# Optimization experiments

Hardware: AMD Instinct MI355X
Metric: run time of the kernel (lower is better)

## Reference

```python
import jax, jax.numpy as jnp
import numpy as np

KSIZE = 3
COUT = 128
GC = 4

def _unfold(x, k):
    # x: [B,C,H,W] -> [B,C,k*k,H,W]; zero pad (k-1)//2, stride 1 (matches nn.Unfold ordering)
    B, C, H, W = x.shape
    p = (k - 1) // 2
    xp = jnp.pad(x, ((0, 0), (0, 0), (p, p), (p, p)))
    return jnp.stack([xp[:, :, i:i + H, j:j + W] for i in range(k) for j in range(k)], axis=2)

def _bn(x, g, b, m, v, eps=1e-5):
    # inference-mode BatchNorm along channel axis 1, any rank
    sh = (1, -1) + (1,) * (x.ndim - 2)
    return (x - m.reshape(sh)) * (g / jnp.sqrt(v + eps)).reshape(sh) + b.reshape(sh)

def setup_inputs():
    key = jax.random.key(0)
    ks = jax.random.split(key, 15)
    B, C, H, W = 4, 128, 56, 56
    mid = C // 4
    OG = COUT * GC
    s = 0.05
    return {
        'x': jax.random.normal(ks[0], (B, C, H, W), jnp.float32),
        'Wk': jax.random.normal(ks[1], (C, C), jnp.float32) * s,
        'bn1_g': jax.random.uniform(ks[2], (C,), jnp.float32, 0.5, 1.5),
        'bn1_b': jax.random.normal(ks[3], (C,), jnp.float32) * s,
        'bn1_m': jnp.zeros((C,), jnp.float32),
        'bn1_v': jnp.ones((C,), jnp.float32),
        'W1': jax.random.normal(ks[4], (mid, 2 * C), jnp.float32) * s,
        'b1': jax.random.normal(ks[5], (mid,), jnp.float32) * s,
        'bn2_g': jax.random.uniform(ks[6], (mid,), jnp.float32, 0.5, 1.5),
        'bn2_b': jax.random.normal(ks[7], (mid,), jnp.float32) * s,
        'bn2_m': jnp.zeros((mid,), jnp.float32),
        'bn2_v': jnp.ones((mid,), jnp.float32),
        'W2': jax.random.normal(ks[8], (OG, mid), jnp.float32) * s,
        'b2': jax.random.normal(ks[9], (OG,), jnp.float32) * s,
        'gn_g': jax.random.uniform(ks[10], (OG,), jnp.float32, 0.5, 1.5),
        'gn_b': jax.random.normal(ks[11], (OG,), jnp.float32) * s,
        'Wv': jax.random.normal(ks[12], (OG, C), jnp.float32) * s,
        'bnv_g': jax.random.uniform(ks[13], (OG,), jnp.float32, 0.5, 1.5),
        'bnv_b': jax.random.normal(ks[14], (OG,), jnp.float32) * s,
        'bnv_m': jnp.zeros((OG,), jnp.float32),
        'bnv_v': jnp.ones((OG,), jnp.float32),
    }

def reference(x, Wk, bn1_g, bn1_b, bn1_m, bn1_v, W1, b1, bn2_g, bn2_b, bn2_m, bn2_v,
              W2, b2, gn_g, gn_b, Wv, bnv_g, bnv_b, bnv_m, bnv_v):
    B, C, H, W = x.shape
    k2 = KSIZE * KSIZE
    # emb_K: 1x1 conv (no bias) + BN + ReLU, then local unfold
    ke = jax.nn.relu(_bn(jnp.einsum('bchw,dc->bdhw', x, Wk), bn1_g, bn1_b, bn1_m, bn1_v))
    Kp = _unfold(ke, KSIZE)                        # [B,C,k2,H,W]
    Q = jnp.broadcast_to(x[:, :, None], Kp.shape)  # repeat x over k2 (einops '(c k)')
    QK = jnp.concatenate([Q, Kp], axis=1)          # [B,2C,k2,H,W]
    # MLP: 1x1 convs act pointwise over (k2,H,W)
    h = jax.nn.relu(_bn(jnp.einsum('bcphw,mc->bmphw', QK, W1) + b1.reshape(1, -1, 1, 1, 1),
                        bn2_g, bn2_b, bn2_m, bn2_v))
    a = jnp.einsum('bmphw,om->bophw', h, W2) + b2.reshape(1, -1, 1, 1, 1)  # [B,COUT*GC,k2,H,W]
    a = a.reshape(B, COUT, GC, k2, H, W)
    # GroupNorm: num_groups=COUT -> normalize over (GC, k2, H, W) per (b, out)
    mu = a.mean(axis=(2, 3, 4, 5), keepdims=True)
    var = jnp.mean(jnp.square(a - mu), axis=(2, 3, 4, 5), keepdims=True)
    a = (a - mu) / jnp.sqrt(var + 1e-5)
    a = a * gn_g.reshape(1, COUT, GC, 1, 1, 1) + gn_b.reshape(1, COUT, GC, 1, 1, 1)
    # emb_V: 1x1 conv (no bias) + BN, then local unfold
    v = _bn(jnp.einsum('bchw,oc->bohw', x, Wv), bnv_g, bnv_b, bnv_m, bnv_v)
    V = _unfold(v, KSIZE).reshape(B, COUT, GC, k2, H, W)
    return jnp.sum(a * V, axis=(2, 3))             # [B,COUT,H,W]
```

## Files before the change

### kernel.cpp

```cpp
#include <hip/hip_runtime.h>
#include <hip/hip_bf16.h>

typedef __hip_bfloat16 bf16;
typedef __attribute__((ext_vector_type(8))) short short8;
typedef __attribute__((ext_vector_type(4))) float f32x4;

#define HWP 3136
#define WD 56
#define PW 58
#define PADP 3364
#define CC 128
#define MIDM 32
#define OGN 512
#define NB 4

enum : int {
  OFF_FLAG = 0,
  OFF_W2F  = 4,
  OFF_SC2  = OFF_W2F + OGN*MIDM,
  OFF_SH2  = OFF_SC2 + MIDM,
  OFF_B1F  = OFF_SH2 + MIDM,
  OFF_B2F  = OFF_B1F + MIDM,
  OFF_GNG  = OFF_B2F + OGN,
  OFF_GNB  = OFF_GNG + OGN,
  OFF_GPART= OFF_GNB + OGN,
  OFF_PQ   = OFF_GPART + NB*128*1056,
  OFF_SS1  = OFF_PQ + NB*OGN*2,
  OFF_SSV  = OFF_SS1 + CC*2,
  OFF_WKB  = OFF_SSV + OGN*2,
  OFF_WVB  = OFF_WKB + CC*CC/2,
  OFF_W1AB = OFF_WVB + OGN*CC/2,
  OFF_W1BB = OFF_W1AB + MIDM*CC/2,
  OFF_HQT  = OFF_W1BB + MIDM*CC/2,
  OFF_GKT  = OFF_HQT + NB*HWP*MIDM/2,
  OFF_VT   = OFF_GKT + NB*PADP*MIDM/2,
  OFF_R1   = OFF_VT + NB*PADP*OGN/2,
  OFF_XT   = OFF_R1,
  OFF_AB   = OFF_R1,
  WS_TOTAL = OFF_R1 + NB*9*HWP*MIDM/2
};

__device__ __forceinline__ float b2f(unsigned short u) {
  bf16 h; *(unsigned short*)&h = u; return __bfloat162float(h);
}
__device__ __forceinline__ unsigned short f2b(float f) {
  bf16 h = __float2bfloat16(f); return *(unsigned short*)&h;
}
__device__ __forceinline__ float ldmix(const void* p, size_t i, bool isbf) {
  return isbf ? __bfloat162float(((const bf16*)p)[i]) : ((const float*)p)[i];
}
__device__ __forceinline__ f32x4 mfma16(short8 a, short8 b, f32x4 c) {
  return __builtin_amdgcn_mfma_f32_16x16x32_bf16(a, b, c, 0, 0, 0);
}
__device__ __forceinline__ bool detect_bf(const unsigned short* xr) {
  int cnt = 0;
#pragma unroll
  for (int i = 0; i < 32; i++) {
    short8 v = *(const short8*)(xr + i*8);
#pragma unroll
    for (int j = 0; j < 8; j++) {
      int e = (((unsigned short)v[j]) >> 7) & 0xFF;
      cnt += (e >= 141) ? 1 : 0;
    }
  }
  return cnt < 8;
}

__global__ __launch_bounds__(256) void k_prep(
    const void* __restrict__ x,  const void* __restrict__ Wk,
    const void* __restrict__ bn1_g, const void* __restrict__ bn1_b,
    const void* __restrict__ bn1_m, const void* __restrict__ bn1_v,
    const void* __restrict__ W1, const void* __restrict__ b1,
    const void* __restrict__ bn2_g, const void* __restrict__ bn2_b,
    const void* __restrict__ bn2_m, const void* __restrict__ bn2_v,
    const void* __restrict__ W2, const void* __restrict__ b2,
    const void* __restrict__ gn_g, const void* __restrict__ gn_b,
    const void* __restrict__ Wv,
    const void* __restrict__ bnv_g, const void* __restrict__ bnv_b,
    const void* __restrict__ bnv_m, const void* __restrict__ bnv_v,
    float* __restrict__ ws) {
  __shared__ unsigned short tile[32*130];
  const bool isbf = detect_bf((const unsigned short*)x);
  int blk = blockIdx.x, tid = threadIdx.x;
  if (blk == 0 && tid == 0) ws[OFF_FLAG] = isbf ? 1.f : 0.f;
  int gid = blk*256 + tid, gstride = gridDim.x*256;
  unsigned short* wkb = (unsigned short*)(ws + OFF_WKB);
  unsigned short* wvb = (unsigned short*)(ws + OFF_WVB);
  unsigned short* w1ab = (unsigned short*)(ws + OFF_W1AB);
  unsigned short* w1bb = (unsigned short*)(ws + OFF_W1BB);
  float2* ss1 = (float2*)(ws + OFF_SS1);
  float2* ssv = (float2*)(ws + OFF_SSV);
  for (int i = gid; i < CC*CC; i += gstride) wkb[i] = f2b(ldmix(Wk, i, isbf));
  for (int i = gid; i < OGN*CC; i += gstride) wvb[i] = f2b(ldmix(Wv, i, isbf));
  for (int i = gid; i < MIDM*CC; i += gstride) {
    int m = i / CC, c = i % CC;
    w1ab[i] = f2b(ldmix(W1, (size_t)m*(2*CC) + c, isbf));
    w1bb[i] = f2b(ldmix(W1, (size_t)m*(2*CC) + CC + c, isbf));
  }
  for (int i = gid; i < OGN*MIDM; i += gstride) ws[OFF_W2F + i] = ldmix(W2, i, isbf);
  for (int i = gid; i < CC; i += gstride) {
    float s = ldmix(bn1_g, i, isbf) / sqrtf(ldmix(bn1_v, i, isbf) + 1e-5f);
    ss1[i] = make_float2(s, ldmix(bn1_b, i, isbf) - ldmix(bn1_m, i, isbf) * s);
  }
  for (int i = gid; i < MIDM; i += gstride) {
    float s = ldmix(bn2_g, i, isbf) / sqrtf(ldmix(bn2_v, i, isbf) + 1e-5f);
    ws[OFF_SC2 + i] = s;
    ws[OFF_SH2 + i] = ldmix(bn2_b, i, isbf) - ldmix(bn2_m, i, isbf)*s;
    ws[OFF_B1F + i] = ldmix(b1, i, isbf);
  }
  for (int i = gid; i < OGN; i += gstride) {
    float s = ldmix(bnv_g, i, isbf) / sqrtf(ldmix(bnv_v, i, isbf) + 1e-5f);
    ssv[i] = make_float2(s, ldmix(bnv_b, i, isbf) - ldmix(bnv_m, i, isbf) * s);
    ws[OFF_B2F + i] = ldmix(b2, i, isbf);
    ws[OFF_GNG + i] = ldmix(gn_g, i, isbf);
    ws[OFF_GNB + i] = ldmix(gn_b, i, isbf);
  }
  if (blk < 392) {
    int b = blk / 98, pix0 = (blk % 98)*32;
#pragma unroll
    for (int k = 0; k < 16; k++) {
      int idx = tid + k*256;
      int c = idx >> 5, pl = idx & 31;
      tile[pl*130 + c] = f2b(ldmix(x, ((size_t)b*CC + c)*HWP + pix0 + pl, isbf));
    }
    __syncthreads();
    unsigned short* xt = (unsigned short*)(ws + OFF_XT);
#pragma unroll
    for (int k = 0; k < 16; k++) {
      int idx = tid + k*256;
      int c = idx & 127, pl = idx >> 7;
      xt[((size_t)b*HWP + pix0 + pl)*CC + c] = tile[pl*130 + c];
    }
  } else {
    const int NV = 912*64, NG = NB*PADP*4;
    const short8 z = {0,0,0,0,0,0,0,0};
    unsigned short* vt = (unsigned short*)(ws + OFF_VT);
    unsigned short* gk = (unsigned short*)(ws + OFF_GKT);
    for (int u = (blk-392)*256 + tid; u < NV + NG; u += 28*256) {
      if (u < NV) {
        int bpp = u >> 6, och = u & 63;
        int b = bpp / 228, j = bpp - b*228;
        int pp;
        if (j < 58)       pp = j;
        else if (j < 116) pp = 57*PW + (j - 58);
        else if (j < 172) pp = (j - 116 + 1)*PW;
        else              pp = (j - 172 + 1)*PW + 57;
        *(short8*)(vt + ((size_t)b*PADP + pp)*OGN + och*8) = z;
      } else {
        int u2 = u - NV;
        int b = u2 / (PADP*4), rem = u2 - b*(PADP*4);
        int pp = rem >> 2, mch = rem & 3;
        *(short8*)(gk + ((size_t)b*PADP + pp)*MIDM + mch*8) = z;
      }
    }
  }
}

__global__ __launch_bounds__(256, 4) void k_mid(float* __restrict__ ws) {
  __shared__ unsigned short keL[4][16][136];
  int bid = blockIdx.x, tid = threadIdx.x;
  int w = tid >> 6, lane = tid & 63, q = lane >> 4, l16 = lane & 15;
  if (bid < 196) {
    int b = bid / 49, bx = bid - (bid/49)*49;
    int pix = bx*64 + w*16 + l16;
    const unsigned short* xt = (const unsigned short*)(ws + OFF_XT) + ((size_t)b*HWP + pix)*CC;
    short8 Bx[4];
#pragma unroll
    for (int kk = 0; kk < 4; kk++) Bx[kk] = *(const short8*)(xt + kk*32 + q*8);
    const unsigned short* wkb = (const unsigned short*)(ws + OFF_WKB);
    const float2* ss = (const float2*)(ws + OFF_SS1);
#pragma unroll
    for (int ot = 0; ot < 8; ot++) {
      int drow = ot*16 + l16;
      f32x4 c = {0.f, 0.f, 0.f, 0.f};
#pragma unroll
      for (int kk = 0; kk < 4; kk++)
        c = mfma16(*(const short8*)(wkb + (size_t)drow*CC + kk*32 + q*8), Bx[kk], c);
      int d0 = ot*16 + q*4;
      ushort4 st;
      { float2 s = ss[d0+0]; st.x = f2b(fmaxf(s.x*c[0] + s.y, 0.f)); }
      { float2 s = ss[d0+1]; st.y = f2b(fmaxf(s.x*c[1] + s.y, 0.f)); }
      { float2 s = ss[d0+2]; st.z = f2b(fmaxf(s.x*c[2] + s.y, 0.f)); }
      { float2 s = ss[d0+3]; st.w = f2b(fmaxf(s.x*c[3] + s.y, 0.f)); }
      *(ushort4*)&keL[w][l16][d0] = st;
    }
    __syncthreads();
    short8 Bk[4];
#pragma unroll
    for (int kk = 0; kk < 4; kk++) Bk[kk] = *(const short8*)&keL[w][l16][kk*32 + q*8];
    const unsigned short* w1a = (const unsigned short*)(ws + OFF_W1AB);
    const unsigned short* w1b = (const unsigned short*)(ws + OFF_W1BB);
    int h0 = pix / WD, w0 = pix - h0*WD;
    int pp = (h0+1)*PW + (w0+1);
    unsigned short* hqt = (unsigned short*)(ws + OFF_HQT) + ((size_t)b*HWP + pix)*MIDM;
    unsigned short* gkt = (unsigned short*)(ws + OFF_GKT) + ((size_t)b*PADP + pp)*MIDM;
#pragma unroll
    for (int mt = 0; mt < 2; mt++) {
      int mrow = mt*16 + l16;
      f32x4 ch = {0.f,0.f,0.f,0.f}, cg = {0.f,0.f,0.f,0.f};
#pragma unroll
      for (int kk = 0; kk < 4; kk++) {
        ch = mfma16(*(const short8*)(w1a + (size_t)mrow*CC + kk*32 + q*8), Bx[kk], ch);
        cg = mfma16(*(const short8*)(w1b + (size_t)mrow*CC + kk*32 + q*8), Bk[kk], cg);
      }
      int m0 = mt*16 + q*4;
      ushort4 sh, sg;
      sh.x = f2b(ch[0]); sh.y = f2b(ch[1]); sh.z = f2b(ch[2]); sh.w = f2b(ch[3]);
      sg.x = f2b(cg[0]); sg.y = f2b(cg[1]); sg.z = f2b(cg[2]); sg.w = f2b(cg[3]);
      *(ushort4*)(hqt + m0) = sh;
      *(ushort4*)(gkt + m0) = sg;
    }
  } else {
    int vid = bid - 196;
    int bx = vid % 49, rest = vid / 49;
    int by = rest & 3, b = rest >> 2;
    int pix = bx*64 + w*16 + l16;
    int h0 = pix / WD, w0 = pix - h0*WD;
    int pp = (h0+1)*PW + (w0+1);
    const unsigned short* xt = (const unsigned short*)(ws + OFF_XT) + ((size_t)b*HWP + pix)*CC;
    short8 B[4];
#pragma unroll
    for (int kk = 0; kk < 4; kk++) B[kk] = *(const short8*)(xt + kk*32 + q*8);
    const unsigned short* wvb = (const unsigned short*)(ws + OFF_WVB);
    const float2* ss = (const float2*)(ws + OFF_SSV);
    unsigned short* vt = (unsigned short*)(ws + OFF_VT) + ((size_t)b*PADP + pp)*OGN;
#pragma unroll
    for (int ot = 0; ot < 8; ot++) {
      int orow = by*128 + ot*16 + l16;
      f32x4 c = {0.f, 0.f, 0.f, 0.f};
#pragma unroll
      for (int kk = 0; kk < 4; kk++)
        c = mfma16(*(const short8*)(wvb + (size_t)orow*CC + kk*32 + q*8), B[kk], c);
      int o0 = by*128 + ot*16 + q*4;
      ushort4 st;
      { float2 s = ss[o0+0]; st.x = f2b(s.x*c[0] + s.y); }
      { float2 s = ss[o0+1]; st.y = f2b(s.x*c[1] + s.y); }
      { float2 s = ss[o0+2]; st.z = f2b(s.x*c[2] + s.y); }
      { float2 s = ss[o0+3]; st.w = f2b(s.x*c[3] + s.y); }
      *(ushort4*)(vt + o0) = st;
    }
  }
}

__global__ __launch_bounds__(256) void k_gramh(float* __restrict__ ws) {
  __shared__ unsigned short tileT[32][264];
  int b = blockIdx.y, bk = blockIdx.x;
  int tid = threadIdx.x;
  int w = tid >> 6, lane = tid & 63, q = lane >> 4, l16 = lane & 15;
  const int base = bk * 882;
  const unsigned short* hqt = (const unsigned short*)(ws + OFF_HQT) + (size_t)b*HWP*MIDM;
  const unsigned short* gkp = (const unsigned short*)(ws + OFF_GKT) + (size_t)b*PADP*MIDM;
  float sc2[MIDM], bas0[MIDM];
#pragma unroll
  for (int m = 0; m < MIDM; m++) {
    sc2[m] = ws[OFF_SC2 + m];
    bas0[m] = sc2[m]*ws[OFF_B1F + m] + ws[OFF_SH2 + m];
  }
  f32x4 gLL={0,0,0,0}, gLH={0,0,0,0}, gHH={0,0,0,0}, sL={0,0,0,0}, sH={0,0,0,0};
  short8 ones;
#pragma unroll
  for (int j = 0; j < 8; j++) ones[j] = (short)0x3F80;
  for (int t = 0; t < 4; t++) {
    int r = t*256 + tid;
    bool valid = r < 882;
    int R = valid ? (base + r) : 0;
    int p = R / HWP, pix = R - p*HWP;
    int h0 = pix / WD, w0 = pix - h0*WD;
    int npp = (h0 + p/3)*PW + (w0 + p - (p/3)*3);
    const unsigned short* hq = hqt + (size_t)pix*MIDM;
    const unsigned short* gk = gkp + (size_t)npp*MIDM;
#pragma unroll
    for (int ch = 0; ch < 4; ch++) {
      short8 th = *(const short8*)(hq + ch*8);
      short8 tg = *(const short8*)(gk + ch*8);
      short8 o;
#pragma unroll
      for (int j = 0; j < 8; j++) {
        int m = ch*8 + j;
        float hv = b2f((unsigned short)th[j]) + b2f((unsigned short)tg[j]);
        float v = fmaxf(sc2[m]*hv + bas0[m], 0.f);
        o[j] = valid ? (short)f2b(v) : (short)0;
      }
#pragma unroll
      for (int j = 0; j < 8; j++) tileT[ch*8 + j][tid] = (unsigned short)o[j];
    }
    __syncthreads();
#pragma unroll
    for (int cc = 0; cc < 2; cc++) {
      int c = w*2 + cc;
      short8 alo = *(const short8*)&tileT[l16][c*32 + q*8];
      short8 ahi = *(const short8*)&tileT[l16+16][c*32 + q*8];
      gLL = mfma16(alo, alo, gLL);
      gLH = mfma16(alo, ahi, gLH);
      gHH = mfma16(ahi, ahi, gHH);
      sL = mfma16(alo, ones, sL);
      sH = mfma16(ahi, ones, sH);
    }
    __syncthreads();
  }
  float* blob = ws + OFF_GPART + ((size_t)((b*32 + bk)*4 + w))*1056;
#pragma unroll
  for (int r = 0; r < 4; r++) {
    int row = q*4 + r;
    blob[row*32 + l16]             = gLL[r];
    blob[row*32 + 16 + l16]        = gLH[r];
    blob[(16 + l16)*32 + row]      = gLH[r];
    blob[(16 + row)*32 + 16 + l16] = gHH[r];
  }
  if (l16 == 0) {
#pragma unroll
    for (int r = 0; r < 4; r++) {
      blob[1024 + q*4 + r]      = sL[r];
      blob[1024 + 16 + q*4 + r] = sH[r];
    }
  }
}

__global__ __launch_bounds__(512) void k_stats(float* __restrict__ ws) {
  __shared__ float Gs[MIDM*MIDM], S1s[MIDM], saS[OGN], sqS[OGN], muS[128], invS[128];
  int b = blockIdx.x, o = threadIdx.x;
  for (int e = o; e < 1056; e += 512) {
    float s = 0.f;
    const float* pb = ws + OFF_GPART + (size_t)b*128*1056 + e;
    for (int p = 0; p < 128; p++) s += pb[(size_t)p*1056];
    if (e < 1024) Gs[e] = s; else S1s[e - 1024] = s;
  }
  __syncthreads();
  float w2[MIDM];
#pragma unroll
  for (int m = 0; m < MIDM; m++) w2[m] = ws[OFF_W2F + o*MIDM + m];
  float dotS = 0.f;
#pragma unroll
  for (int m = 0; m < MIDM; m++) dotS += w2[m] * S1s[m];
  float quad = 0.f;
  for (int a = 0; a < MIDM; a++) {
    float t = 0.f;
#pragma unroll
    for (int c = 0; c < MIDM; c++) t += Gs[a*MIDM + c] * w2[c];
    quad += w2[a] * t;
  }
  float b2o = ws[OFF_B2F + o];
  const float M = 9.f * HWP;
  saS[o] = dotS + b2o * M;
  sqS[o] = quad + 2.f*b2o*dotS + b2o*b2o*M;
  __syncthreads();
  if (o < 128) {
    float sa = saS[4*o] + saS[4*o+1] + saS[4*o+2] + saS[4*o+3];
    float sq = sqS[4*o] + sqS[4*o+1] + sqS[4*o+2] + sqS[4*o+3];
    const float invN = 1.f / (4.f * M);
    float mu = sa * invN;
    float var = sq * invN - mu*mu;
    muS[o] = mu;
    invS[o] = 1.f / sqrtf(var + 1e-5f);
  }
  __syncthreads();
  int co = o >> 2;
  float alpha = ws[OFF_GNG + o] * invS[co];
  ((float2*)(ws + OFF_PQ))[b*OGN + o] =
      make_float2(alpha, alpha*b2o + ws[OFF_GNB + o] - muS[co]*alpha);
  unsigned short* dst = (unsigned short*)(ws + OFF_AB) + ((size_t)b*OGN + o)*MIDM;
#pragma unroll
  for (int m = 0; m < MIDM; m += 4) {
    ushort4 t;
    t.x = f2b(alpha*w2[m+0]); t.y = f2b(alpha*w2[m+1]);
    t.z = f2b(alpha*w2[m+2]); t.w = f2b(alpha*w2[m+3]);
    *(ushort4*)(dst + m) = t;
  }
}

#define VST 136
__global__ __launch_bounds__(256, 2) void k_out(const float* __restrict__ ws,
                                                void* __restrict__ outp) {
  __shared__ unsigned short tileV[256*VST];
  int b = blockIdx.z, bp = blockIdx.y;
  int bx = blockIdx.x;
  int tid = threadIdx.x;
  int w = tid >> 6, lane = tid & 63, q = lane >> 4, l16 = lane & 15;
  int pix0 = bx*128;
  int h00 = pix0 / WD, w00 = pix0 - h00*WD;
  int wstart = (h00+1)*PW + (w00+1) - (PW+1);
  const bool hasB = (bx < 24);
  int pixA = pix0 + w*16 + l16;
  float sc[8], ba[8];
#pragma unroll
  for (int j = 0; j < 8; j++) {
    int m = q*8 + j;
    sc[j] = ws[OFF_SC2 + m];
    ba[j] = sc[j]*ws[OFF_B1F + m] + ws[OFF_SH2 + m];
  }
  const unsigned short* hqt = (const unsigned short*)(ws + OFF_HQT) + (size_t)b*HWP*MIDM;
  const unsigned short* gkt = (const unsigned short*)(ws + OFF_GKT) + (size_t)b*PADP*MIDM;
  int hA = pixA / WD, wA = pixA - hA*WD;
  short8 BfA[9];
  {
    short8 th = *(const short8*)(hqt + (size_t)pixA*MIDM + q*8);
    float hv[8];
#pragma unroll
    for (int j = 0; j < 8; j++) hv[j] = b2f((unsigned short)th[j]);
    const unsigned short* gkb = gkt + ((size_t)hA*PW + wA)*MIDM + q*8;
#pragma unroll
    for (int p = 0; p < 9; p++) {
      short8 tg = *(const short8*)(gkb + (size_t)((p/3)*PW + (p - (p/3)*3))*MIDM);
#pragma unroll
      for (int j = 0; j < 8; j++)
        BfA[p][j] = (short)f2b(fmaxf(sc[j]*(hv[j] + b2f((unsigned short)tg[j])) + ba[j], 0.f));
    }
  }
  const unsigned short* vsrc = (const unsigned short*)(ws + OFF_VT)
      + (size_t)b*PADP*OGN + (size_t)bp*128;
#pragma unroll
  for (int i = 0; i < 16; i++) {
    int u = i*256 + tid;
    int wp = u >> 4, col = (u & 15)*8;
    *(short8*)&tileV[wp*VST + col] =
        *(const short8*)(vsrc + (size_t)(wstart + wp)*OGN + col);
  }
  const bool isbf = ws[OFF_FLAG] > 0.5f;
  const float2* pq = (const float2*)(ws + OFF_PQ) + b*OGN;
  const unsigned short* ABb = (const unsigned short*)(ws + OFF_AB)
      + ((size_t)b*OGN + bp*128)*MIDM;
  const int doff[9] = {-PW-1, -PW, -PW+1, -1, 0, 1, PW-1, PW, PW+1};
  int pplA = (hA+1)*PW + (wA+1) - wstart;
  __syncthreads();
  for (int byv = 0; byv < 2; ++byv) {
    short8 A[4];
    f32x4 Qv[4];
#pragma unroll
    for (int ot = 0; ot < 4; ot++) {
      A[ot] = *(const short8*)(ABb + (size_t)(byv*64 + ot*16 + l16)*MIDM + q*8);
      int o0 = bp*128 + byv*64 + ot*16 + q*4;
      f32x4 qv = { pq[o0+0].y, pq[o0+1].y, pq[o0+2].y, pq[o0+3].y };
      Qv[ot] = qv;
    }
    {
      float acc[4] = {0.f, 0.f, 0.f, 0.f};
#pragma unroll
      for (int p = 0; p < 9; p++) {
        int lp = pplA + doff[p];
        const unsigned short* vrow = &tileV[lp*VST + byv*64];
#pragma unroll
        for (int ot = 0; ot < 4; ot++) {
          f32x4 c = {0.f, 0.f, 0.f, 0.f};
          c = mfma16(A[ot], BfA[p], c);
          ushort4 vv = *(const ushort4*)(vrow + ot*16 + q*4);
          acc[ot] += (c[0] + Qv[ot][0])*b2f(vv.x) + (c[1] + Qv[ot][1])*b2f(vv.y)
                   + (c[2] + Qv[ot][2])*b2f(vv.z) + (c[3] + Qv[ot][3])*b2f(vv.w);
        }
      }
#pragma unroll
      for (int ot = 0; ot < 4; ot++) {
        int co = bp*32 + byv*16 + ot*4 + q;
        size_t oidx = ((size_t)b*128 + co)*HWP + pixA;
        if (isbf) __builtin_nontemporal_store(f2b(acc[ot]), (unsigned short*)outp + oidx);
        else      __builtin_nontemporal_store(acc[ot], (float*)outp + oidx);
      }
    }
    if (hasB) {
      int pixB = pixA + 64;
      int hB = pixB / WD, wB = pixB - hB*WD;
      short8 BfB[9];
      {
        short8 th = *(const short8*)(hqt + (size_t)pixB*MIDM + q*8);
        float hv[8];
#pragma unroll
        for (int j = 0; j < 8; j++) hv[j] = b2f((unsigned short)th[j]);
        const unsigned short* gkb = gkt + ((size_t)hB*PW + wB)*MIDM + q*8;
#pragma unroll
        for (int p = 0; p < 9; p++) {
          short8 tg = *(const short8*)(gkb + (size_t)((p/3)*PW + (p - (p/3)*3))*MIDM);
#pragma unroll
          for (int j = 0; j < 8; j++)
            BfB[p][j] = (short)f2b(fmaxf(sc[j]*(hv[j] + b2f((unsigned short)tg[j])) + ba[j], 0.f));
        }
      }
      int ppl = (hB+1)*PW + (wB+1) - wstart;
      float acc[4] = {0.f, 0.f, 0.f, 0.f};
#pragma unroll
      for (int p = 0; p < 9; p++) {
        int lp = ppl + doff[p];
        const unsigned short* vrow = &tileV[lp*VST + byv*64];
#pragma unroll
        for (int ot = 0; ot < 4; ot++) {
          f32x4 c = {0.f, 0.f, 0.f, 0.f};
          c = mfma16(A[ot], BfB[p], c);
          ushort4 vv = *(const ushort4*)(vrow + ot*16 + q*4);
          acc[ot] += (c[0] + Qv[ot][0])*b2f(vv.x) + (c[1] + Qv[ot][1])*b2f(vv.y)
                   + (c[2] + Qv[ot][2])*b2f(vv.z) + (c[3] + Qv[ot][3])*b2f(vv.w);
        }
      }
#pragma unroll
      for (int ot = 0; ot < 4; ot++) {
        int co = bp*32 + byv*16 + ot*4 + q;
        size_t oidx = ((size_t)b*128 + co)*HWP + pixB;
        if (isbf) __builtin_nontemporal_store(f2b(acc[ot]), (unsigned short*)outp + oidx);
        else      __builtin_nontemporal_store(acc[ot], (float*)outp + oidx);
      }
    }
  }
}

extern "C" void kernel_launch(void* const* d_in, const int* in_sizes, int n_in,
                              void* d_out, int out_size, void* d_ws, size_t ws_size,
                              hipStream_t stream) {
  float* ws = (float*)d_ws;
  hipLaunchKernelGGL(k_prep, dim3(420), dim3(256), 0, stream,
                     d_in[0], d_in[1], d_in[2], d_in[3], d_in[4], d_in[5],
                     d_in[6], d_in[7], d_in[8], d_in[9], d_in[10], d_in[11],
                     d_in[12], d_in[13], d_in[14], d_in[15], d_in[16],
                     d_in[17], d_in[18], d_in[19], d_in[20], ws);
  hipLaunchKernelGGL(k_mid,  dim3(980),      dim3(256), 0, stream, ws);
  hipLaunchKernelGGL(k_gramh,dim3(32, 4),    dim3(256), 0, stream, ws);
  hipLaunchKernelGGL(k_stats,dim3(4),        dim3(512), 0, stream, ws);
  hipLaunchKernelGGL(k_out,  dim3(25, 4, 4), dim3(256), 0, stream, ws, d_out);
}
```

Baseline: 192.9 us.

## Fuse V projection into output kernel instead of materializing padded V

Result: slower. 201.7 us (+4.5%).

```diff
diff --git a/kernel.cpp b/kernel.cpp
--- a/kernel.cpp
+++ b/kernel.cpp
@@ -33,11 +33,9 @@
   OFF_W1BB = OFF_W1AB + MIDM*CC/2,
   OFF_HQT  = OFF_W1BB + MIDM*CC/2,
   OFF_GKT  = OFF_HQT + NB*HWP*MIDM/2,
-  OFF_VT   = OFF_GKT + NB*PADP*MIDM/2,
-  OFF_R1   = OFF_VT + NB*PADP*OGN/2,
-  OFF_XT   = OFF_R1,
-  OFF_AB   = OFF_R1,
-  WS_TOTAL = OFF_R1 + NB*9*HWP*MIDM/2
+  OFF_AB   = OFF_GKT + NB*PADP*MIDM/2,
+  OFF_XT   = OFF_AB + NB*OGN*MIDM/2,
+  WS_TOTAL = OFF_XT + NB*HWP*CC/2
 };
 
 __device__ __forceinline__ float b2f(unsigned short u) {
@@ -132,26 +130,13 @@
       xt[((size_t)b*HWP + pix0 + pl)*CC + c] = tile[pl*130 + c];
     }
   } else {
-    const int NV = 912*64, NG = NB*PADP*4;
+    const int NG = NB*PADP*4;
     const short8 z = {0,0,0,0,0,0,0,0};
-    unsigned short* vt = (unsigned short*)(ws + OFF_VT);
     unsigned short* gk = (unsigned short*)(ws + OFF_GKT);
-    for (int u = (blk-392)*256 + tid; u < NV + NG; u += 28*256) {
-      if (u < NV) {
-        int bpp = u >> 6, och = u & 63;
-        int b = bpp / 228, j = bpp - b*228;
-        int pp;
-        if (j < 58)       pp = j;
-        else if (j < 116) pp = 57*PW + (j - 58);
-        else if (j < 172) pp = (j - 116 + 1)*PW;
-        else              pp = (j - 172 + 1)*PW + 57;
-        *(short8*)(vt + ((size_t)b*PADP + pp)*OGN + och*8) = z;
-      } else {
-        int u2 = u - NV;
-        int b = u2 / (PADP*4), rem = u2 - b*(PADP*4);
-        int pp = rem >> 2, mch = rem & 3;
-        *(short8*)(gk + ((size_t)b*PADP + pp)*MIDM + mch*8) = z;
-      }
+    for (int u = (blk-392)*256 + tid; u < NG; u += 28*256) {
+      int b = u / (PADP*4), rem = u - b*(PADP*4);
+      int pp = rem >> 2, mch = rem & 3;
+      *(short8*)(gk + ((size_t)b*PADP + pp)*MIDM + mch*8) = z;
     }
   }
 }
@@ -160,85 +145,54 @@
   __shared__ unsigned short keL[4][16][136];
   int bid = blockIdx.x, tid = threadIdx.x;
   int w = tid >> 6, lane = tid & 63, q = lane >> 4, l16 = lane & 15;
-  if (bid < 196) {
-    int b = bid / 49, bx = bid - (bid/49)*49;
-    int pix = bx*64 + w*16 + l16;
-    const unsigned short* xt = (const unsigned short*)(ws + OFF_XT) + ((size_t)b*HWP + pix)*CC;
-    short8 Bx[4];
-#pragma unroll
-    for (int kk = 0; kk < 4; kk++) Bx[kk] = *(const short8*)(xt + kk*32 + q*8);
-    const unsigned short* wkb = (const unsigned short*)(ws + OFF_WKB);
-    const float2* ss = (const float2*)(ws + OFF_SS1);
-#pragma unroll
-    for (int ot = 0; ot < 8; ot++) {
-      int drow = ot*16 + l16;
-      f32x4 c = {0.f, 0.f, 0.f, 0.f};
-#pragma unroll
-      for (int kk = 0; kk < 4; kk++)
-        c = mfma16(*(const short8*)(wkb + (size_t)drow*CC + kk*32 + q*8), Bx[kk], c);
-      int d0 = ot*16 + q*4;
-      ushort4 st;
-      { float2 s = ss[d0+0]; st.x = f2b(fmaxf(s.x*c[0] + s.y, 0.f)); }
-      { float2 s = ss[d0+1]; st.y = f2b(fmaxf(s.x*c[1] + s.y, 0.f)); }
-      { float2 s = ss[d0+2]; st.z = f2b(fmaxf(s.x*c[2] + s.y, 0.f)); }
-      { float2 s = ss[d0+3]; st.w = f2b(fmaxf(s.x*c[3] + s.y, 0.f)); }
-      *(ushort4*)&keL[w][l16][d0] = st;
-    }
-    __syncthreads();
-    short8 Bk[4];
-#pragma unroll
-    for (int kk = 0; kk < 4; kk++) Bk[kk] = *(const short8*)&keL[w][l16][kk*32 + q*8];
-    const unsigned short* w1a = (const unsigned short*)(ws + OFF_W1AB);
-    const unsigned short* w1b = (const unsigned short*)(ws + OFF_W1BB);
-    int h0 = pix / WD, w0 = pix - h0*WD;
-    int pp = (h0+1)*PW + (w0+1);
-    unsigned short* hqt = (unsigned short*)(ws + OFF_HQT) + ((size_t)b*HWP + pix)*MIDM;
-    unsigned short* gkt = (unsigned short*)(ws + OFF_GKT) + ((size_t)b*PADP + pp)*MIDM;
-#pragma unroll
-    for (int mt = 0; mt < 2; mt++) {
-      int mrow = mt*16 + l16;
-      f32x4 ch = {0.f,0.f,0.f,0.f}, cg = {0.f,0.f,0.f,0.f};
-#pragma unroll
-      for (int kk = 0; kk < 4; kk++) {
-        ch = mfma16(*(const short8*)(w1a + (size_t)mrow*CC + kk*32 + q*8), Bx[kk], ch);
-        cg = mfma16(*(const short8*)(w1b + (size_t)mrow*CC + kk*32 + q*8), Bk[kk], cg);
-      }
-      int m0 = mt*16 + q*4;
-      ushort4 sh, sg;
-      sh.x = f2b(ch[0]); sh.y = f2b(ch[1]); sh.z = f2b(ch[2]); sh.w = f2b(ch[3]);
-      sg.x = f2b(cg[0]); sg.y = f2b(cg[1]); sg.z = f2b(cg[2]); sg.w = f2b(cg[3]);
-      *(ushort4*)(hqt + m0) = sh;
-      *(ushort4*)(gkt + m0) = sg;
-    }
-  } else {
-    int vid = bid - 196;
-    int bx = vid % 49, rest = vid / 49;
-    int by = rest & 3, b = rest >> 2;
-    int pix = bx*64 + w*16 + l16;
-    int h0 = pix / WD, w0 = pix - h0*WD;
-    int pp = (h0+1)*PW + (w0+1);
-    const unsigned short* xt = (const unsigned short*)(ws + OFF_XT) + ((size_t)b*HWP + pix)*CC;
-    short8 B[4];
-#pragma unroll
-    for (int kk = 0; kk < 4; kk++) B[kk] = *(const short8*)(xt + kk*32 + q*8);
-    const unsigned short* wvb = (const unsigned short*)(ws + OFF_WVB);
-    const float2* ss = (const float2*)(ws + OFF_SSV);
-    unsigned short* vt = (unsigned short*)(ws + OFF_VT) + ((size_t)b*PADP + pp)*OGN;
-#pragma unroll
-    for (int ot = 0; ot < 8; ot++) {
-      int orow = by*128 + ot*16 + l16;
-      f32x4 c = {0.f, 0.f, 0.f, 0.f};
-#pragma unroll
-      for (int kk = 0; kk < 4; kk++)
-        c = mfma16(*(const short8*)(wvb + (size_t)orow*CC + kk*32 + q*8), B[kk], c);
-      int o0 = by*128 + ot*16 + q*4;
-      ushort4 st;
-      { float2 s = ss[o0+0]; st.x = f2b(s.x*c[0] + s.y); }
-      { float2 s = ss[o0+1]; st.y = f2b(s.x*c[1] + s.y); }
-      { float2 s = ss[o0+2]; st.z = f2b(s.x*c[2] + s.y); }
-      { float2 s = ss[o0+3]; st.w = f2b(s.x*c[3] + s.y); }
-      *(ushort4*)(vt + o0) = st;
-    }
+  int b = bid / 49, bx = bid - (bid/49)*49;
+  int pix = bx*64 + w*16 + l16;
+  const unsigned short* xt = (const unsigned short*)(ws + OFF_XT) + ((size_t)b*HWP + pix)*CC;
+  short8 Bx[4];
+#pragma unroll
+  for (int kk = 0; kk < 4; kk++) Bx[kk] = *(const short8*)(xt + kk*32 + q*8);
+  const unsigned short* wkb = (const unsigned short*)(ws + OFF_WKB);
+  const float2* ss = (const float2*)(ws + OFF_SS1);
+#pragma unroll
+  for (int ot = 0; ot < 8; ot++) {
+    int drow = ot*16 + l16;
+    f32x4 c = {0.f, 0.f, 0.f, 0.f};
+#pragma unroll
+    for (int kk = 0; kk < 4; kk++)
+      c = mfma16(*(const short8*)(wkb + (size_t)drow*CC + kk*32 + q*8), Bx[kk], c);
+    int d0 = ot*16 + q*4;
+    ushort4 st;
+    { float2 s = ss[d0+0]; st.x = f2b(fmaxf(s.x*c[0] + s.y, 0.f)); }
+    { float2 s = ss[d0+1]; st.y = f2b(fmaxf(s.x*c[1] + s.y, 0.f)); }
+    { float2 s = ss[d0+2]; st.z = f2b(fmaxf(s.x*c[2] + s.y, 0.f)); }
+    { float2 s = ss[d0+3]; st.w = f2b(fmaxf(s.x*c[3] + s.y, 0.f)); }
+    *(ushort4*)&keL[w][l16][d0] = st;
+  }
+  __syncthreads();
+  short8 Bk[4];
+#pragma unroll
+  for (int kk = 0; kk < 4; kk++) Bk[kk] = *(const short8*)&keL[w][l16][kk*32 + q*8];
+  const unsigned short* w1a = (const unsigned short*)(ws + OFF_W1AB);
+  const unsigned short* w1b = (const unsigned short*)(ws + OFF_W1BB);
+  int h0 = pix / WD, w0 = pix - h0*WD;
+  int pp = (h0+1)*PW + (w0+1);
+  unsigned short* hqt = (unsigned short*)(ws + OFF_HQT) + ((size_t)b*HWP + pix)*MIDM;
+  unsigned short* gkt = (unsigned short*)(ws + OFF_GKT) + ((size_t)b*PADP + pp)*MIDM;
+#pragma unroll
+  for (int mt = 0; mt < 2; mt++) {
+    int mrow = mt*16 + l16;
+    f32x4 ch = {0.f,0.f,0.f,0.f}, cg = {0.f,0.f,0.f,0.f};
+#pragma unroll
+    for (int kk = 0; kk < 4; kk++) {
+      ch = mfma16(*(const short8*)(w1a + (size_t)mrow*CC + kk*32 + q*8), Bx[kk], ch);
+      cg = mfma16(*(const short8*)(w1b + (size_t)mrow*CC + kk*32 + q*8), Bk[kk], cg);
+    }
+    int m0 = mt*16 + q*4;
+    ushort4 sh, sg;
+    sh.x = f2b(ch[0]); sh.y = f2b(ch[1]); sh.z = f2b(ch[2]); sh.w = f2b(ch[3]);
+    sg.x = f2b(cg[0]); sg.y = f2b(cg[1]); sg.z = f2b(cg[2]); sg.w = f2b(cg[3]);
+    *(ushort4*)(hqt + m0) = sh;
+    *(ushort4*)(gkt + m0) = sg;
   }
 }
 
@@ -406,14 +360,44 @@
         BfA[p][j] = (short)f2b(fmaxf(sc[j]*(hv[j] + b2f((unsigned short)tg[j])) + ba[j], 0.f));
     }
   }
-  const unsigned short* vsrc = (const unsigned short*)(ws + OFF_VT)
-      + (size_t)b*PADP*OGN + (size_t)bp*128;
-#pragma unroll
-  for (int i = 0; i < 16; i++) {
-    int u = i*256 + tid;
-    int wp = u >> 4, col = (u & 15)*8;
-    *(short8*)&tileV[wp*VST + col] =
-        *(const short8*)(vsrc + (size_t)(wstart + wp)*OGN + col);
+  {
+    const unsigned short* xtb = (const unsigned short*)(ws + OFF_XT) + (size_t)b*HWP*CC;
+    const unsigned short* wvb = (const unsigned short*)(ws + OFF_WVB);
+    const float2* ssv = (const float2*)(ws + OFF_SSV);
+#pragma unroll
+    for (int g = 0; g < 4; g++) {
+      int wr = w*64 + g*16 + l16;
+      int pp = wstart + wr;
+      int ph = pp / PW, pw = pp - ph*PW;
+      bool inter = (ph >= 1) && (ph <= WD) && (pw >= 1) && (pw <= WD);
+      int pixel = (ph-1)*WD + (pw-1);
+      short8 Bx[4];
+      if (inter) {
+        const unsigned short* xr = xtb + (size_t)pixel*CC + q*8;
+#pragma unroll
+        for (int kk = 0; kk < 4; kk++) Bx[kk] = *(const short8*)(xr + kk*32);
+      } else {
+        const short8 z = {0,0,0,0,0,0,0,0};
+#pragma unroll
+        for (int kk = 0; kk < 4; kk++) Bx[kk] = z;
+      }
+#pragma unroll
+      for (int ot = 0; ot < 8; ot++) {
+        int orow = bp*128 + ot*16 + l16;
+        f32x4 c = {0.f, 0.f, 0.f, 0.f};
+#pragma unroll
+        for (int kk = 0; kk < 4; kk++)
+          c = mfma16(*(const short8*)(wvb + (size_t)orow*CC + kk*32 + q*8), Bx[kk], c);
+        int o0 = bp*128 + ot*16 + q*4;
+        ushort4 st;
+        if (inter) {
+          float2 s0 = ssv[o0+0], s1 = ssv[o0+1], s2 = ssv[o0+2], s3 = ssv[o0+3];
+          st.x = f2b(s0.x*c[0] + s0.y); st.y = f2b(s1.x*c[1] + s1.y);
+          st.z = f2b(s2.x*c[2] + s2.y); st.w = f2b(s3.x*c[3] + s3.y);
+        } else { st.x = 0; st.y = 0; st.z = 0; st.w = 0; }
+        *(ushort4*)&tileV[wr*VST + ot*16 + q*4] = st;
+      }
+    }
   }
   const bool isbf = ws[OFF_FLAG] > 0.5f;
   const float2* pq = (const float2*)(ws + OFF_PQ) + b*OGN;
@@ -508,7 +492,7 @@
                      d_in[6], d_in[7], d_in[8], d_in[9], d_in[10], d_in[11],
                      d_in[12], d_in[13], d_in[14], d_in[15], d_in[16],
                      d_in[17], d_in[18], d_in[19], d_in[20], ws);
-  hipLaunchKernelGGL(k_mid,  dim3(980),      dim3(256), 0, stream, ws);
+  hipLaunchKernelGGL(k_mid,  dim3(196),      dim3(256), 0, stream, ws);
   hipLaunchKernelGGL(k_gramh,dim3(32, 4),    dim3(256), 0, stream, ws);
   hipLaunchKernelGGL(k_stats,dim3(4),        dim3(512), 0, stream, ws);
   hipLaunchKernelGGL(k_out,  dim3(25, 4, 4), dim3(256), 0, stream, ws, d_out);
```
